# Optimization experiments

Hardware: AMD Instinct MI355X
Metric: run time of the kernel (lower is better)

## Reference

```python
import jax, jax.numpy as jnp
import numpy as np

LMAX = 4
DSH = (LMAX + 1) ** 2          # 25 spherical-harmonic coefficients
C = 32                          # channels per degree l
N = 10000                       # nodes
E = 160000                      # edges
FC = 64                         # fc_len_in (radial/edge scalar feature dim)

# flattened (l,m) index = l^2 + l + m
IDX0 = np.array([l * l + l for l in range(LMAX + 1)])               # m = 0 coeffs
POS = {m: np.array([l * l + l + m for l in range(m, LMAX + 1)]) for m in range(1, LMAX + 1)}
NEG = {m: np.array([l * l + l - m for l in range(m, LMAX + 1)]) for m in range(1, LMAX + 1)}
L_OF_IDX = np.concatenate([np.full(2 * l + 1, l) for l in range(LMAX + 1)])  # degree of each coeff


def setup_inputs() -> dict:
    key = jax.random.key(0)
    ks = jax.random.split(key, 20)
    inp = {
        "x": jax.random.normal(ks[0], (N, DSH, C), jnp.float32),
        "wigner": jax.random.normal(ks[1], (E, DSH, DSH), jnp.float32) * 0.2,
        "edge_fc": jax.random.normal(ks[2], (E, FC), jnp.float32),
        "edge_src": jax.random.randint(ks[3], (E,), 0, N),
        "edge_dst": jax.random.randint(ks[4], (E,), 0, N),
    }
    # per-m SO(2) block weights
    d0 = (LMAX + 1) * C
    inp["w0"] = jax.random.normal(ks[5], (d0, d0), jnp.float32) / np.sqrt(d0)
    k = 6
    for m in range(1, LMAX + 1):
        dm = (LMAX + 1 - m) * C
        inp[f"w{m}r"] = jax.random.normal(ks[k], (dm, dm), jnp.float32) / np.sqrt(dm); k += 1
        inp[f"w{m}i"] = jax.random.normal(ks[k], (dm, dm), jnp.float32) / np.sqrt(dm); k += 1
    # radial/cfconv network producing per-(degree, channel) scales
    inp["fc_w"] = jax.random.normal(ks[k], (FC, (LMAX + 1) * C), jnp.float32) / np.sqrt(FC)
    inp["fc_b"] = jnp.zeros(((LMAX + 1) * C,), jnp.float32)
    return inp


def reference(x, wigner, edge_fc, edge_src, edge_dst,
              w0, w1r, w1i, w2r, w2i, w3r, w3i, w4r, w4i, fc_w, fc_b):
    Wr = {1: w1r, 2: w2r, 3: w3r, 4: w4r}
    Wi = {1: w1i, 2: w2i, 3: w3i, 4: w4i}
    # gather node features to edges and rotate into edge-aligned frame
    xe = x[edge_src]                                   # [E, 25, C]
    xr = jnp.einsum('eij,ejc->eic', wigner, xe)        # [E, 25, C]
    Ee = xr.shape[0]
    y = jnp.zeros_like(xr)
    # m = 0 block: real linear over stacked-l channels
    x0 = xr[:, IDX0, :].reshape(Ee, -1)                # [E, 5*C]
    y = y.at[:, IDX0, :].set((x0 @ w0).reshape(Ee, LMAX + 1, C))
    # m > 0 blocks: SO(2) complex-style mixing
    for m in range(1, LMAX + 1):
        pos, neg = POS[m], NEG[m]
        Lm = len(pos)
        xp = xr[:, pos, :].reshape(Ee, -1)             # [E, Lm*C]
        xn = xr[:, neg, :].reshape(Ee, -1)
        yp = xp @ Wr[m] - xn @ Wi[m]
        yn = xp @ Wi[m] + xn @ Wr[m]
        y = y.at[:, pos, :].set(yp.reshape(Ee, Lm, C))
        y = y.at[:, neg, :].set(yn.reshape(Ee, Lm, C))
    # cfconv: per-edge radial scaling, one scalar per (degree, channel)
    scale = jax.nn.silu(edge_fc @ fc_w + fc_b).reshape(Ee, LMAX + 1, C)
    y = y * scale[:, L_OF_IDX, :]
    # rotate back (Wigner D is orthogonal -> transpose is inverse)
    yb = jnp.einsum('eji,ejc->eic', wigner, y)
    # scatter-aggregate messages to destination nodes
    return jax.ops.segment_sum(yb, edge_dst, num_segments=N)
```

## Files before the change

kernel.cpp:

```cpp
#include <hip/hip_runtime.h>

typedef __attribute__((ext_vector_type(8))) short short8;
typedef __attribute__((ext_vector_type(4))) short short4v;
typedef __attribute__((ext_vector_type(4))) float f32x4;

#define MFMA16(a,b,c) __builtin_amdgcn_mfma_f32_16x16x32_bf16((a),(b),(c),0,0,0)

__device__ __align__(16) short g_wt[117760];
__device__ __align__(16) short g_wtf[148480];
__device__ __align__(16) short g_fcwt[10240];

struct K2Tab {
  int   fbase[50];
  int   pboff[50][8];
  short acoeff[50][8];
  short len[50];
  short dm[50];
  short ut[50];
  short ocoeff[50];
  short lsc[50];
  short co16[50];
  short pu[290];
  short pk[290];
};

constexpr K2Tab make_k2tab() {
  K2Tab T{};
  const int P[5][5]  = {{0,2,6,12,20},{3,7,13,21,0},{8,14,22,0,0},{15,23,0,0,0},{24,0,0,0,0}};
  const int Ng[5][5] = {{0,0,0,0,0},{1,5,11,19,0},{4,10,18,0,0},{9,17,0,0,0},{16,0,0,0,0}};
  const int WR[5]  = {0, 25600, 74752, 102400, 114688};
  const int WI[5]  = {0, 41984, 83968, 106496, 115712};
  const int NWI[5] = {0, 58368, 93184, 110592, 116736};
  const int ms[9]  = {1,1,2,2,0,3,3,4,4};
  const int hs[9]  = {0,1,0,1,0,0,1,0,1};
  const int ntc[9] = {8,8,6,6,10,4,4,2,2};
  int u = 0, fb = 0, np = 0;
  for (int g = 0; g < 9; ++g) {
    const int m = ms[g], h = hs[g];
    const int dm = (m == 0) ? 160 : (5 - m) * 32;
    const int lm = (m == 0) ? 5 : (5 - m);
    const int len = (m == 0) ? 5 : 2 * lm;
    const int b1 = (m == 0) ? 0 : ((h == 0) ? WR[m] : WI[m]);
    const int b2 = (m == 0) ? 0 : ((h == 0) ? NWI[m] : WR[m]);
    for (int tt = 0; tt < ntc[g]; ++tt, ++u) {
      T.dm[u] = (short)dm; T.len[u] = (short)len; T.ut[u] = (short)tt;
      const int lo = tt >> 1;
      T.ocoeff[u] = (short)((m == 0) ? P[0][lo] : ((h == 0) ? P[m][lo] : Ng[m][lo]));
      T.lsc[u] = (short)(m + lo);
      T.co16[u] = (short)((tt & 1) * 16);
      T.fbase[u] = fb;
      for (int k = 0; k < len; ++k) {
        int bb, ac;
        if (m == 0)      { bb = k * 32;            ac = P[0][k]; }
        else if (k < lm) { bb = b1 + k * 32;       ac = P[m][k]; }
        else             { bb = b2 + (k - lm) * 32; ac = Ng[m][k - lm]; }
        T.pboff[u][k] = bb; T.acoeff[u][k] = (short)ac;
        T.pu[np] = (short)u; T.pk[np] = (short)k; ++np;
      }
      fb += len * 512;
    }
  }
  return T;
}
__constant__ K2Tab c_kt = make_k2tab();

__device__ __forceinline__ short f2bf(float f) {
  unsigned u = __float_as_uint(f);
  u += 0x7FFFu + ((u >> 16) & 1u);
  return (short)(u >> 16);
}

__global__ void prep_weights(const float* __restrict__ w0,
    const float* __restrict__ w1r, const float* __restrict__ w1i,
    const float* __restrict__ w2r, const float* __restrict__ w2i,
    const float* __restrict__ w3r, const float* __restrict__ w3i,
    const float* __restrict__ w4r, const float* __restrict__ w4i,
    const float* __restrict__ fcw) {
  int idx = blockIdx.x * 256 + threadIdx.x;
  if (idx >= 128000) return;
  if (idx >= 117760) {
    int local = idx - 117760;
    int n = local >> 6, k = local & 63;
    g_fcwt[local] = f2bf(fcw[k * 160 + n]);
    return;
  }
  int off, dm; const float* src; bool neg = false;
  if (idx < 25600)       { off = 0;      dm = 160; src = w0;  }
  else if (idx < 41984)  { off = 25600;  dm = 128; src = w1r; }
  else if (idx < 58368)  { off = 41984;  dm = 128; src = w1i; }
  else if (idx < 74752)  { off = 58368;  dm = 128; src = w1i; neg = true; }
  else if (idx < 83968)  { off = 74752;  dm = 96;  src = w2r; }
  else if (idx < 93184)  { off = 83968;  dm = 96;  src = w2i; }
  else if (idx < 102400) { off = 93184;  dm = 96;  src = w2i; neg = true; }
  else if (idx < 106496) { off = 102400; dm = 64;  src = w3r; }
  else if (idx < 110592) { off = 106496; dm = 64;  src = w3i; }
  else if (idx < 114688) { off = 110592; dm = 64;  src = w3i; neg = true; }
  else if (idx < 115712) { off = 114688; dm = 32;  src = w4r; }
  else if (idx < 116736) { off = 115712; dm = 32;  src = w4i; }
  else                   { off = 116736; dm = 32;  src = w4i; neg = true; }
  int local = idx - off;
  int n = local / dm, k = local - n * dm;
  float v = src[k * dm + n];
  g_wt[idx] = f2bf(neg ? -v : v);
}

__global__ void prep_frags() {
  int i = blockIdx.x * 256 + threadIdx.x;
  if (i >= 290 * 512) return;
  int p = i >> 9;
  int w = i & 511;
  int lane = w >> 3, j = w & 7;
  int l15 = lane & 15, lg = lane >> 4;
  int u = c_kt.pu[p], k = c_kt.pk[p];
  int col = (int)c_kt.ut[u] * 16 + l15;
  g_wtf[i] = g_wt[c_kt.pboff[u][k] + col * (int)c_kt.dm[u] + lg * 8 + j];
}

__global__ void hist_kernel(const int* __restrict__ edst, int* __restrict__ cnt, int E) {
  int i = blockIdx.x * 256 + threadIdx.x;
  if (i < E) atomicAdd(&cnt[edst[i]], 1);
}

__global__ __launch_bounds__(1024) void scan_kernel(
    const int* __restrict__ cnt, int* __restrict__ cursor, int N) {
  __shared__ int s[1024];
  const int t = threadIdx.x;
  int v[10]; int sum = 0;
  #pragma unroll
  for (int k = 0; k < 10; ++k) {
    int i = t * 10 + k;
    v[k] = (i < N) ? cnt[i] : 0;
    sum += v[k];
  }
  s[t] = sum;
  __syncthreads();
  for (int d = 1; d < 1024; d <<= 1) {
    int add = (t >= d) ? s[t - d] : 0;
    __syncthreads();
    s[t] += add;
    __syncthreads();
  }
  int prefix = s[t] - sum;
  #pragma unroll
  for (int k = 0; k < 10; ++k) {
    int i = t * 10 + k;
    if (i < N) cursor[i] = prefix;
    prefix += v[k];
  }
}

__global__ void scatter_kernel(const int* __restrict__ edst, int* __restrict__ cursor,
                               int* __restrict__ order, int E) {
  int i = blockIdx.x * 256 + threadIdx.x;
  if (i < E) {
    int p = atomicAdd(&cursor[edst[i]], 1);
    order[p] = i;
  }
}

__global__ __launch_bounds__(256, 6) void k1_rotate(
    const float* __restrict__ x, const float* __restrict__ wig,
    const int* __restrict__ esrc, const int* __restrict__ order,
    short* __restrict__ xr, int E)
{
  __shared__ __align__(16) short s_xe[8 * 1304];
  __shared__ int s_og[8], s_src[8];

  const int tid = threadIdx.x;
  const int lane = tid & 63;
  const int wid = tid >> 6;
  const int l15 = lane & 15;
  const int lg  = lane >> 4;
  const int e0  = blockIdx.x * 8;

  for (int o = tid; o < 5216; o += 256) ((int*)s_xe)[o] = 0;
  if (tid < 8) {
    int idx = min(e0 + tid, E - 1);
    int og = order[idx];
    s_og[tid] = og;
    s_src[tid] = esrc[og];
  }
  __syncthreads();

  for (int o = tid; o < 6400; o += 256) {
    int e = o / 800, q = o - e * 800;
    s_xe[e * 1304 + (q & 31) * 40 + (q >> 5)] = f2bf(x[(size_t)s_src[e] * 800 + q]);
  }
  __syncthreads();

  #pragma unroll
  for (int i = 0; i < 2; ++i) {
    const int e = wid * 2 + i;
    const int slot = e0 + e;
    if (slot >= E) continue;
    const short* xeb = s_xe + e * 1304;
    const float* wp = wig + (size_t)s_og[e] * 625;
    short8 a0 = *(const short8*)(xeb + l15 * 40 + lg * 8);
    short8 a1 = *(const short8*)(xeb + (16 + l15) * 40 + lg * 8);
    short8 b0, b1;
    const int r1 = min(16 + l15, 24);
    #pragma unroll
    for (int j = 0; j < 8; ++j) {
      const int k = lg * 8 + j;
      const int kc = min(k, 24);
      const short v0 = f2bf(wp[l15 * 25 + kc]);
      const short v1 = f2bf(wp[r1 * 25 + kc]);
      b0[j] = (k < 25) ? v0 : (short)0;
      b1[j] = (k < 25) ? v1 : (short)0;
    }
    f32x4 d00 = {0.f,0.f,0.f,0.f}, d01 = {0.f,0.f,0.f,0.f};
    f32x4 d10 = {0.f,0.f,0.f,0.f}, d11 = {0.f,0.f,0.f,0.f};
    d00 = MFMA16(a0, b0, d00);
    d01 = MFMA16(a0, b1, d01);
    d10 = MFMA16(a1, b0, d10);
    d11 = MFMA16(a1, b1, d11);
    short* xp = xr + (size_t)slot * 800;
    short4v v;
    v[0]=f2bf(d00[0]); v[1]=f2bf(d00[1]); v[2]=f2bf(d00[2]); v[3]=f2bf(d00[3]);
    *(short4v*)(xp + l15 * 32 + lg * 4) = v;
    v[0]=f2bf(d10[0]); v[1]=f2bf(d10[1]); v[2]=f2bf(d10[2]); v[3]=f2bf(d10[3]);
    *(short4v*)(xp + l15 * 32 + 16 + lg * 4) = v;
    if (l15 < 9) {
      v[0]=f2bf(d01[0]); v[1]=f2bf(d01[1]); v[2]=f2bf(d01[2]); v[3]=f2bf(d01[3]);
      *(short4v*)(xp + (16 + l15) * 32 + lg * 4) = v;
      v[0]=f2bf(d11[0]); v[1]=f2bf(d11[1]); v[2]=f2bf(d11[2]); v[3]=f2bf(d11[3]);
      *(short4v*)(xp + (16 + l15) * 32 + 16 + lg * 4) = v;
    }
  }
}

__global__ __launch_bounds__(512, 4) void k2_mix(
    short* __restrict__ xr, const float* __restrict__ efc,
    const int* __restrict__ order, const float* __restrict__ fcb, int E)
{
  __shared__ __align__(16) short s_x[32 * 808];
  __shared__ _Float16 s_sc[32 * 168];

  const int tid = threadIdx.x;
  const int lane = tid & 63;
  const int wid = tid >> 6;
  const int l15 = lane & 15;
  const int lg  = lane >> 4;
  const int koff = lg * 8;
  const int e0  = blockIdx.x * 32;

  for (int o = tid; o < 3200; o += 512) {
    int e = o / 100, r = o - e * 100;
    int slot = min(e0 + e, E - 1);
    *(short8*)(s_x + e * 808 + r * 8) = *(const short8*)(xr + (size_t)slot * 800 + r * 8);
  }

  {
    const int mt = wid >> 2;
    const int ge = order[min(e0 + mt * 16 + l15, E - 1)];
    const float* ep = efc + (size_t)ge * 64;
    float4 fa = *(const float4*)(ep + lg * 8);
    float4 fb = *(const float4*)(ep + lg * 8 + 4);
    float4 fc = *(const float4*)(ep + 32 + lg * 8);
    float4 fd = *(const float4*)(ep + 32 + lg * 8 + 4);
    short8 af0, af1;
    af0[0]=f2bf(fa.x); af0[1]=f2bf(fa.y); af0[2]=f2bf(fa.z); af0[3]=f2bf(fa.w);
    af0[4]=f2bf(fb.x); af0[5]=f2bf(fb.y); af0[6]=f2bf(fb.z); af0[7]=f2bf(fb.w);
    af1[0]=f2bf(fc.x); af1[1]=f2bf(fc.y); af1[2]=f2bf(fc.z); af1[3]=f2bf(fc.w);
    af1[4]=f2bf(fd.x); af1[5]=f2bf(fd.y); af1[6]=f2bf(fd.z); af1[7]=f2bf(fd.w);
    for (int nt = (wid & 3); nt < 10; nt += 4) {
      const int f = nt * 16 + l15;
      const short* bp = g_fcwt + f * 64 + lg * 8;
      short8 b0 = *(const short8*)(bp);
      short8 b1 = *(const short8*)(bp + 32);
      f32x4 acc = {0.f, 0.f, 0.f, 0.f};
      acc = MFMA16(af0, b0, acc);
      acc = MFMA16(af1, b1, acc);
      float bias = fcb[f];
      #pragma unroll
      for (int r = 0; r < 4; ++r) {
        float vv = acc[r] + bias;
        s_sc[(mt * 16 + lg * 4 + r) * 168 + (f >> 5) * 33 + (f & 31)] =
            (_Float16)(vv / (1.f + __expf(-vv)));
      }
    }
  }
  __syncthreads();

  for (int u = wid; u < 50; u += 8) {
    const int len = c_kt.len[u];
    const short* Bp = g_wtf + c_kt.fbase[u] + lane * 8;
    short8 B[8];
    #pragma unroll 8
    for (int k = 0; k < 8; ++k) {
      if (k < len) B[k] = *(const short8*)(Bp + (k << 9));
    }
    const int co = c_kt.co16[u] + l15;
    const int oc = c_kt.ocoeff[u];
    const int ls = c_kt.lsc[u];
    #pragma unroll 2
    for (int mt = 0; mt < 2; ++mt) {
      const short* xl = s_x + (mt * 16 + l15) * 808 + koff;
      f32x4 acc0 = {0.f,0.f,0.f,0.f}, acc1 = {0.f,0.f,0.f,0.f};
      #pragma unroll 8
      for (int k = 0; k < 8; ++k) {
        if (k < len) {
          short8 a = *(const short8*)(xl + (int)c_kt.acoeff[u][k] * 32);
          if (k & 1) acc1 = MFMA16(a, B[k], acc1);
          else       acc0 = MFMA16(a, B[k], acc0);
        }
      }
      f32x4 acc = acc0 + acc1;
      #pragma unroll
      for (int r = 0; r < 4; ++r) {
        const int el = mt * 16 + lg * 4 + r;
        const int slot = e0 + el;
        if (slot < E) {
          float sc = (float)s_sc[el * 168 + ls * 33 + co];
          xr[(size_t)slot * 800 + oc * 32 + co] = f2bf(acc[r] * sc);
        }
      }
    }
  }
}

__global__ __launch_bounds__(256, 5) void k3_back(
    const short* __restrict__ y, const float* __restrict__ wig,
    const int* __restrict__ edst, const int* __restrict__ order,
    const int* __restrict__ cnt, float* __restrict__ out, int E)
{
  __shared__ __align__(16) char sumem[27136];
  __shared__ int s_meta[64];
  short* s_y  = (short*)sumem;
  float* yb_s = (float*)sumem;

  const int tid = threadIdx.x;
  const int lane = tid & 63;
  const int wid = tid >> 6;
  const int l15 = lane & 15;
  const int lg  = lane >> 4;
  const int e0  = blockIdx.x * 8;

  for (int o = tid; o < 5216; o += 256) ((int*)sumem)[o] = 0;
  if (tid < 8) {
    int idx = e0 + tid;
    bool v = idx < E;
    int og = order[v ? idx : 0];
    s_meta[tid] = og;
    s_meta[16 + tid] = v ? edst[og] : -1;
  }
  __syncthreads();

  if (wid == 0) {
    int dj = (lane < 8) ? s_meta[16 + lane] : -1;
    bool valid = (lane < 8) && (dj >= 0);
    bool is_start = valid && (lane == 0 || dj != s_meta[16 + lane - 1]);
    unsigned long long vm = __ballot(valid);
    unsigned long long sm = __ballot(is_start);
    int nv = __popcll(vm);
    int ng = __popcll(sm);
    if (lane == 0) s_meta[24] = ng;
    if ((int)lane < ng) {
      int s = -1, c = -1;
      for (int b = 0; b < 8; ++b) { if ((sm >> b) & 1) { ++c; if (c == (int)lane) { s = b; break; } } }
      int e_ = nv;
      for (int b = s + 1; b < 8; ++b) if ((sm >> b) & 1) { e_ = b; break; }
      int d = s_meta[16 + s];
      s_meta[25 + lane] = d;
      s_meta[33 + lane] = s;
      s_meta[41 + lane] = e_;
      s_meta[49 + lane] = ((e_ - s) == cnt[d]) ? 1 : 0;
    }
  }
  for (int o = tid; o < 800; o += 256) {
    int e = o / 100, r = o - e * 100;
    int slot = min(e0 + e, E - 1);
    int q = r * 8;
    *(short8*)(s_y + e * 1304 + (q >> 5) * 40 + (q & 31)) =
        *(const short8*)(y + (size_t)slot * 800 + q);
  }
  __syncthreads();

  f32x4 r00[2], r01[2], r10[2], r11[2];
  #pragma unroll
  for (int i = 0; i < 2; ++i) {
    const int e = wid * 2 + i;
    const short* yb = s_y + e * 1304 + lg * 8 * 40;
    const float* wp = wig + (size_t)s_meta[e] * 625;
    short8 a0, a1, b0, b1;
    const int c2 = min(16 + l15, 24);
    #pragma unroll 8
    for (int j = 0; j < 8; ++j) {
      a0[j] = yb[j * 40 + l15];
      a1[j] = yb[j * 40 + 16 + l15];
      const int k = lg * 8 + j;
      const int kc = min(k, 24);
      const short v0 = f2bf(wp[kc * 25 + l15]);
      const short v1 = f2bf(wp[kc * 25 + c2]);
      b0[j] = (k < 25) ? v0 : (short)0;
      b1[j] = (k < 25) ? v1 : (short)0;
    }
    f32x4 d00 = {0.f,0.f,0.f,0.f}, d01 = {0.f,0.f,0.f,0.f};
    f32x4 d10 = {0.f,0.f,0.f,0.f}, d11 = {0.f,0.f,0.f,0.f};
    d00 = MFMA16(a0, b0, d00);
    d01 = MFMA16(a0, b1, d01);
    d10 = MFMA16(a1, b0, d10);
    d11 = MFMA16(a1, b1, d11);
    r00[i] = d00; r01[i] = d01; r10[i] = d10; r11[i] = d11;
  }
  __syncthreads();

  #pragma unroll
  for (int i = 0; i < 2; ++i) {
    const int e = wid * 2 + i;
    float* yb = yb_s + e * 840;
    #pragma unroll 4
    for (int r = 0; r < 4; ++r) {
      yb[l15 * 33 + lg * 4 + r]      = r00[i][r];
      yb[l15 * 33 + 16 + lg * 4 + r] = r10[i][r];
    }
    if (l15 < 9) {
      #pragma unroll 4
      for (int r = 0; r < 4; ++r) {
        yb[(16 + l15) * 33 + lg * 4 + r]      = r01[i][r];
        yb[(16 + l15) * 33 + 16 + lg * 4 + r] = r11[i][r];
      }
    }
  }
  __syncthreads();

  const int ng = s_meta[24];
  for (int o = tid; o < 800; o += 256) {
    const int yoff = (o >> 5) * 33 + (o & 31);
    for (int g = 0; g < ng; ++g) {
      float sum = 0.f;
      const int gs = s_meta[33 + g], ge = s_meta[41 + g];
      for (int e = gs; e < ge; ++e) sum += yb_s[e * 840 + yoff];
      float* ad = out + (size_t)s_meta[25 + g] * 800 + o;
      if (s_meta[49 + g]) *ad = sum;
      else atomicAdd(ad, sum);
    }
  }
}

extern "C" void kernel_launch(void* const* d_in, const int* in_sizes, int n_in,
                              void* d_out, int out_size, void* d_ws, size_t ws_size,
                              hipStream_t stream) {
  const float* x    = (const float*)d_in[0];
  const float* wigp = (const float*)d_in[1];
  const float* efc  = (const float*)d_in[2];
  const int*   esrc = (const int*)d_in[3];
  const int*   edst = (const int*)d_in[4];
  const float* w0   = (const float*)d_in[5];
  const float* w1r  = (const float*)d_in[6];
  const float* w1i  = (const float*)d_in[7];
  const float* w2r  = (const float*)d_in[8];
  const float* w2i  = (const float*)d_in[9];
  const float* w3r  = (const float*)d_in[10];
  const float* w3i  = (const float*)d_in[11];
  const float* w4r  = (const float*)d_in[12];
  const float* w4i  = (const float*)d_in[13];
  const float* fcw  = (const float*)d_in[14];
  const float* fcb  = (const float*)d_in[15];
  float* out = (float*)d_out;
  const int E = in_sizes[3];
  const int N = out_size / 800;

  int* cnt    = (int*)d_ws;
  int* cursor = cnt + N;
  int* order  = cnt + 2 * N;
  size_t xr_off = (((size_t)(2 * N + E) * 4) + 255) & ~(size_t)255;
  short* xr = (short*)((char*)d_ws + xr_off);

  prep_weights<<<(128000 + 255) / 256, 256, 0, stream>>>(
      w0, w1r, w1i, w2r, w2i, w3r, w3i, w4r, w4i, fcw);
  prep_frags<<<(290 * 512 + 255) / 256, 256, 0, stream>>>();

  hipMemsetAsync(d_out, 0, (size_t)out_size * sizeof(float), stream);
  hipMemsetAsync(cnt, 0, (size_t)N * sizeof(int), stream);

  hist_kernel<<<(E + 255) / 256, 256, 0, stream>>>(edst, cnt, E);
  scan_kernel<<<1, 1024, 0, stream>>>(cnt, cursor, N);
  scatter_kernel<<<(E + 255) / 256, 256, 0, stream>>>(edst, cursor, order, E);

  k1_rotate<<<(E + 7) / 8, 256, 0, stream>>>(x, wigp, esrc, order, xr, E);
  k2_mix<<<(E + 31) / 32, 512, 0, stream>>>(xr, efc, order, fcb, E);
  k3_back<<<(E + 7) / 8, 256, 0, stream>>>(xr, wigp, edst, order, cnt, out, E);
}
```

Measured before the change: 809.4 us.

## Fuse rotation and SO(2) mixing kernels to keep rotated features in LDS

Merges the forward Wigner rotation kernel and the per-m mixing/radial-scale kernel into one kernel that processes 16 edges per 512-thread block. The rotated features stay in shared memory instead of making a bf16 round trip through global memory. The mixing stage now covers a single 16-edge M tile per block, so each B-fragment load is reused across half as many edges, and the larger shared buffer may lower occupancy.

```diff
diff --git a/kernel.cpp b/kernel.cpp
--- a/kernel.cpp
+++ b/kernel.cpp
@@ -158,83 +158,15 @@
   }
 }
 
-__global__ __launch_bounds__(256, 6) void k1_rotate(
+__global__ __launch_bounds__(512, 6) void k12_fused(
     const float* __restrict__ x, const float* __restrict__ wig,
-    const int* __restrict__ esrc, const int* __restrict__ order,
-    short* __restrict__ xr, int E)
+    const float* __restrict__ efc, const int* __restrict__ esrc,
+    const int* __restrict__ order, const float* __restrict__ fcb,
+    short* __restrict__ y, int E)
 {
-  __shared__ __align__(16) short s_xe[8 * 1304];
-  __shared__ int s_og[8], s_src[8];
-
-  const int tid = threadIdx.x;
-  const int lane = tid & 63;
-  const int wid = tid >> 6;
-  const int l15 = lane & 15;
-  const int lg  = lane >> 4;
-  const int e0  = blockIdx.x * 8;
-
-  for (int o = tid; o < 5216; o += 256) ((int*)s_xe)[o] = 0;
-  if (tid < 8) {
-    int idx = min(e0 + tid, E - 1);
-    int og = order[idx];
-    s_og[tid] = og;
-    s_src[tid] = esrc[og];
-  }
-  __syncthreads();
-
-  for (int o = tid; o < 6400; o += 256) {
-    int e = o / 800, q = o - e * 800;
-    s_xe[e * 1304 + (q & 31) * 40 + (q >> 5)] = f2bf(x[(size_t)s_src[e] * 800 + q]);
-  }
-  __syncthreads();
-
-  #pragma unroll
-  for (int i = 0; i < 2; ++i) {
-    const int e = wid * 2 + i;
-    const int slot = e0 + e;
-    if (slot >= E) continue;
-    const short* xeb = s_xe + e * 1304;
-    const float* wp = wig + (size_t)s_og[e] * 625;
-    short8 a0 = *(const short8*)(xeb + l15 * 40 + lg * 8);
-    short8 a1 = *(const short8*)(xeb + (16 + l15) * 40 + lg * 8);
-    short8 b0, b1;
-    const int r1 = min(16 + l15, 24);
-    #pragma unroll
-    for (int j = 0; j < 8; ++j) {
-      const int k = lg * 8 + j;
-      const int kc = min(k, 24);
-      const short v0 = f2bf(wp[l15 * 25 + kc]);
-      const short v1 = f2bf(wp[r1 * 25 + kc]);
-      b0[j] = (k < 25) ? v0 : (short)0;
-      b1[j] = (k < 25) ? v1 : (short)0;
-    }
-    f32x4 d00 = {0.f,0.f,0.f,0.f}, d01 = {0.f,0.f,0.f,0.f};
-    f32x4 d10 = {0.f,0.f,0.f,0.f}, d11 = {0.f,0.f,0.f,0.f};
-    d00 = MFMA16(a0, b0, d00);
-    d01 = MFMA16(a0, b1, d01);
-    d10 = MFMA16(a1, b0, d10);
-    d11 = MFMA16(a1, b1, d11);
-    short* xp = xr + (size_t)slot * 800;
-    short4v v;
-    v[0]=f2bf(d00[0]); v[1]=f2bf(d00[1]); v[2]=f2bf(d00[2]); v[3]=f2bf(d00[3]);
-    *(short4v*)(xp + l15 * 32 + lg * 4) = v;
-    v[0]=f2bf(d10[0]); v[1]=f2bf(d10[1]); v[2]=f2bf(d10[2]); v[3]=f2bf(d10[3]);
-    *(short4v*)(xp + l15 * 32 + 16 + lg * 4) = v;
-    if (l15 < 9) {
-      v[0]=f2bf(d01[0]); v[1]=f2bf(d01[1]); v[2]=f2bf(d01[2]); v[3]=f2bf(d01[3]);
-      *(short4v*)(xp + (16 + l15) * 32 + lg * 4) = v;
-      v[0]=f2bf(d11[0]); v[1]=f2bf(d11[1]); v[2]=f2bf(d11[2]); v[3]=f2bf(d11[3]);
-      *(short4v*)(xp + (16 + l15) * 32 + 16 + lg * 4) = v;
-    }
-  }
-}
-
-__global__ __launch_bounds__(512, 4) void k2_mix(
-    short* __restrict__ xr, const float* __restrict__ efc,
-    const int* __restrict__ order, const float* __restrict__ fcb, int E)
-{
-  __shared__ __align__(16) short s_x[32 * 808];
-  __shared__ _Float16 s_sc[32 * 168];
+  __shared__ __align__(16) short s_buf[16 * 1304];
+  __shared__ _Float16 s_sc[16 * 168];
+  __shared__ int s_meta[32];
 
   const int tid = threadIdx.x;
   const int lane = tid & 63;
@@ -242,17 +174,23 @@
   const int l15 = lane & 15;
   const int lg  = lane >> 4;
   const int koff = lg * 8;
-  const int e0  = blockIdx.x * 32;
-
-  for (int o = tid; o < 3200; o += 512) {
-    int e = o / 100, r = o - e * 100;
-    int slot = min(e0 + e, E - 1);
-    *(short8*)(s_x + e * 808 + r * 8) = *(const short8*)(xr + (size_t)slot * 800 + r * 8);
-  }
-
+  const int e0  = blockIdx.x * 16;
+
+  for (int o = tid; o < 10432; o += 512) ((int*)s_buf)[o] = 0;
+  if (tid < 16) {
+    int idx = min(e0 + tid, E - 1);
+    int og = order[idx];
+    s_meta[tid] = og;
+    s_meta[16 + tid] = esrc[og];
+  }
+  __syncthreads();
+
+  for (int o = tid; o < 12800; o += 512) {
+    int e = o / 800, q = o - e * 800;
+    s_buf[e * 1304 + (q & 31) * 40 + (q >> 5)] = f2bf(x[(size_t)s_meta[16 + e] * 800 + q]);
+  }
   {
-    const int mt = wid >> 2;
-    const int ge = order[min(e0 + mt * 16 + l15, E - 1)];
+    const int ge = s_meta[l15];
     const float* ep = efc + (size_t)ge * 64;
     float4 fa = *(const float4*)(ep + lg * 8);
     float4 fb = *(const float4*)(ep + lg * 8 + 4);
@@ -263,7 +201,7 @@
     af0[4]=f2bf(fb.x); af0[5]=f2bf(fb.y); af0[6]=f2bf(fb.z); af0[7]=f2bf(fb.w);
     af1[0]=f2bf(fc.x); af1[1]=f2bf(fc.y); af1[2]=f2bf(fc.z); af1[3]=f2bf(fc.w);
     af1[4]=f2bf(fd.x); af1[5]=f2bf(fd.y); af1[6]=f2bf(fd.z); af1[7]=f2bf(fd.w);
-    for (int nt = (wid & 3); nt < 10; nt += 4) {
+    for (int nt = wid; nt < 10; nt += 8) {
       const int f = nt * 16 + l15;
       const short* bp = g_fcwt + f * 64 + lg * 8;
       short8 b0 = *(const short8*)(bp);
@@ -275,9 +213,56 @@
       #pragma unroll
       for (int r = 0; r < 4; ++r) {
         float vv = acc[r] + bias;
-        s_sc[(mt * 16 + lg * 4 + r) * 168 + (f >> 5) * 33 + (f & 31)] =
+        s_sc[(lg * 4 + r) * 168 + (f >> 5) * 33 + (f & 31)] =
             (_Float16)(vv / (1.f + __expf(-vv)));
       }
+    }
+  }
+  __syncthreads();
+
+  f32x4 d00[2], d01[2], d10[2], d11[2];
+  #pragma unroll
+  for (int i = 0; i < 2; ++i) {
+    const int e = wid * 2 + i;
+    const short* xeb = s_buf + e * 1304;
+    const float* wp = wig + (size_t)s_meta[e] * 625;
+    short8 a0 = *(const short8*)(xeb + l15 * 40 + koff);
+    short8 a1 = *(const short8*)(xeb + (16 + l15) * 40 + koff);
+    short8 b0, b1;
+    const int r1 = min(16 + l15, 24);
+    #pragma unroll
+    for (int j = 0; j < 8; ++j) {
+      const int k = koff + j;
+      const int kc = min(k, 24);
+      const short v0 = f2bf(wp[l15 * 25 + kc]);
+      const short v1 = f2bf(wp[r1 * 25 + kc]);
+      b0[j] = (k < 25) ? v0 : (short)0;
+      b1[j] = (k < 25) ? v1 : (short)0;
+    }
+    f32x4 t00 = {0.f,0.f,0.f,0.f}, t01 = {0.f,0.f,0.f,0.f};
+    f32x4 t10 = {0.f,0.f,0.f,0.f}, t11 = {0.f,0.f,0.f,0.f};
+    t00 = MFMA16(a0, b0, t00);
+    t01 = MFMA16(a0, b1, t01);
+    t10 = MFMA16(a1, b0, t10);
+    t11 = MFMA16(a1, b1, t11);
+    d00[i] = t00; d01[i] = t01; d10[i] = t10; d11[i] = t11;
+  }
+  __syncthreads();
+
+  #pragma unroll
+  for (int i = 0; i < 2; ++i) {
+    const int e = wid * 2 + i;
+    short* xp = s_buf + e * 1304;
+    short4v v;
+    v[0]=f2bf(d00[i][0]); v[1]=f2bf(d00[i][1]); v[2]=f2bf(d00[i][2]); v[3]=f2bf(d00[i][3]);
+    *(short4v*)(xp + l15 * 32 + lg * 4) = v;
+    v[0]=f2bf(d10[i][0]); v[1]=f2bf(d10[i][1]); v[2]=f2bf(d10[i][2]); v[3]=f2bf(d10[i][3]);
+    *(short4v*)(xp + l15 * 32 + 16 + lg * 4) = v;
+    if (l15 < 9) {
+      v[0]=f2bf(d01[i][0]); v[1]=f2bf(d01[i][1]); v[2]=f2bf(d01[i][2]); v[3]=f2bf(d01[i][3]);
+      *(short4v*)(xp + (16 + l15) * 32 + lg * 4) = v;
+      v[0]=f2bf(d11[i][0]); v[1]=f2bf(d11[i][1]); v[2]=f2bf(d11[i][2]); v[3]=f2bf(d11[i][3]);
+      *(short4v*)(xp + (16 + l15) * 32 + 16 + lg * 4) = v;
     }
   }
   __syncthreads();
@@ -287,33 +272,29 @@
     const short* Bp = g_wtf + c_kt.fbase[u] + lane * 8;
     short8 B[8];
     #pragma unroll 8
-    for (int k = 0; k < 8; ++k) {
+    for (int k = 0; k < 8; ++k)
       if (k < len) B[k] = *(const short8*)(Bp + (k << 9));
-    }
     const int co = c_kt.co16[u] + l15;
     const int oc = c_kt.ocoeff[u];
     const int ls = c_kt.lsc[u];
-    #pragma unroll 2
-    for (int mt = 0; mt < 2; ++mt) {
-      const short* xl = s_x + (mt * 16 + l15) * 808 + koff;
-      f32x4 acc0 = {0.f,0.f,0.f,0.f}, acc1 = {0.f,0.f,0.f,0.f};
-      #pragma unroll 8
-      for (int k = 0; k < 8; ++k) {
-        if (k < len) {
-          short8 a = *(const short8*)(xl + (int)c_kt.acoeff[u][k] * 32);
-          if (k & 1) acc1 = MFMA16(a, B[k], acc1);
-          else       acc0 = MFMA16(a, B[k], acc0);
-        }
+    const short* xl = s_buf + l15 * 1304 + koff;
+    f32x4 acc0 = {0.f,0.f,0.f,0.f}, acc1 = {0.f,0.f,0.f,0.f};
+    #pragma unroll 8
+    for (int k = 0; k < 8; ++k) {
+      if (k < len) {
+        short8 a = *(const short8*)(xl + (int)c_kt.acoeff[u][k] * 32);
+        if (k & 1) acc1 = MFMA16(a, B[k], acc1);
+        else       acc0 = MFMA16(a, B[k], acc0);
       }
-      f32x4 acc = acc0 + acc1;
-      #pragma unroll
-      for (int r = 0; r < 4; ++r) {
-        const int el = mt * 16 + lg * 4 + r;
-        const int slot = e0 + el;
-        if (slot < E) {
-          float sc = (float)s_sc[el * 168 + ls * 33 + co];
-          xr[(size_t)slot * 800 + oc * 32 + co] = f2bf(acc[r] * sc);
-        }
+    }
+    f32x4 acc = acc0 + acc1;
+    #pragma unroll
+    for (int r = 0; r < 4; ++r) {
+      const int el = lg * 4 + r;
+      const int slot = e0 + el;
+      if (slot < E) {
+        float sc = (float)s_sc[el * 168 + ls * 33 + co];
+        y[(size_t)slot * 800 + oc * 32 + co] = f2bf(acc[r] * sc);
       }
     }
   }
@@ -464,8 +445,8 @@
   int* cnt    = (int*)d_ws;
   int* cursor = cnt + N;
   int* order  = cnt + 2 * N;
-  size_t xr_off = (((size_t)(2 * N + E) * 4) + 255) & ~(size_t)255;
-  short* xr = (short*)((char*)d_ws + xr_off);
+  size_t y_off = (((size_t)(2 * N + E) * 4) + 255) & ~(size_t)255;
+  short* yb = (short*)((char*)d_ws + y_off);
 
   prep_weights<<<(128000 + 255) / 256, 256, 0, stream>>>(
       w0, w1r, w1i, w2r, w2i, w3r, w3i, w4r, w4i, fcw);
@@ -478,7 +459,7 @@
   scan_kernel<<<1, 1024, 0, stream>>>(cnt, cursor, N);
   scatter_kernel<<<(E + 255) / 256, 256, 0, stream>>>(edst, cursor, order, E);
 
-  k1_rotate<<<(E + 7) / 8, 256, 0, stream>>>(x, wigp, esrc, order, xr, E);
-  k2_mix<<<(E + 31) / 32, 512, 0, stream>>>(xr, efc, order, fcb, E);
-  k3_back<<<(E + 7) / 8, 256, 0, stream>>>(xr, wigp, edst, order, cnt, out, E);
-}
+  k12_fused<<<(E + 15) / 16, 512, 0, stream>>>(
+      x, wigp, efc, esrc, order, fcb, yb, E);
+  k3_back<<<(E + 7) / 8, 256, 0, stream>>>(yb, wigp, edst, order, cnt, out, E);
+}
```

Result: faster. 783.3 us (-3.2%).
